# Kernel tuning notes

Hardware: AMD Instinct MI355X
Metric: run time of the kernel (lower is better)

## Reference

```python
import jax, jax.numpy as jnp
import numpy as np

N_NODES = 50000
N_EDGES = 800000
NFEAT, NHID, NCLASS = 128, 256, 64


def setup_inputs() -> dict:
    key = jax.random.key(0)
    ks = jax.random.split(key, 8)
    x = jax.random.normal(ks[0], (N_NODES, NFEAT), dtype=jnp.float32)
    edge_index = jax.random.randint(ks[1], (2, N_EDGES), 0, N_NODES, dtype=jnp.int64)
    s1 = 1.0 / np.sqrt(NFEAT)
    s2 = 1.0 / np.sqrt(NHID)
    W1_neigh = jax.random.normal(ks[2], (NFEAT, NHID), dtype=jnp.float32) * s1
    W1_root = jax.random.normal(ks[3], (NFEAT, NHID), dtype=jnp.float32) * s1
    b1 = jnp.zeros((NHID,), dtype=jnp.float32)
    W2_neigh = jax.random.normal(ks[4], (NHID, NCLASS), dtype=jnp.float32) * s2
    W2_root = jax.random.normal(ks[5], (NHID, NCLASS), dtype=jnp.float32) * s2
    b2 = jnp.zeros((NCLASS,), dtype=jnp.float32)
    return {"x": x, "edge_index": edge_index, "W1_neigh": W1_neigh,
            "W1_root": W1_root, "b1": b1, "W2_neigh": W2_neigh,
            "W2_root": W2_root, "b2": b2}


def _sage_conv(h, src, dst, n_nodes, W_neigh, W_root, b):
    # mean aggregation of source features into destination nodes
    msg = h[src]                                                   # [E, d]
    summed = jax.ops.segment_sum(msg, dst, num_segments=n_nodes)   # [N, d]
    cnt = jax.ops.segment_sum(jnp.ones((src.shape[0],), h.dtype), dst,
                              num_segments=n_nodes)                # [N]
    mean = summed / jnp.maximum(cnt, 1.0)[:, None]
    return mean @ W_neigh + h @ W_root + b


def reference(x, edge_index, W1_neigh, W1_root, b1, W2_neigh, W2_root, b2):
    src, dst = edge_index[0], edge_index[1]
    n = x.shape[0]
    h = jax.nn.relu(_sage_conv(x, src, dst, n, W1_neigh, W1_root, b1))
    # dropout is identity in eval mode
    out = _sage_conv(h, src, dst, n, W2_neigh, W2_root, b2)
    return out
```

## Files before the change

### kernel.cpp

```cpp
#include <hip/hip_runtime.h>

#define N_NODES 50000
#define N_EDGES 800000
#define NFEAT   128
#define NHID    256
#define NCLASS  64

#define NPASS 8
#define PASS_W ((N_NODES + NPASS - 1) / NPASS)
#define ECHUNK ((N_EDGES + 255) / 256)
#define ELLCAP 64

#define FILL_B (ECHUNK * NPASS)
#define CVTX_B ((N_NODES * 32 + 255) / 256)
#define CVTW_B (((65536 + 32768) + 255) / 256)

typedef unsigned short u16;
typedef unsigned int   u32;
typedef __attribute__((ext_vector_type(8))) u16   u16x8;
typedef __attribute__((ext_vector_type(8))) short s16x8;
typedef __attribute__((ext_vector_type(4))) float f32x4;

__device__ inline u16 f2bf(float f) {
    u32 u = __float_as_uint(f);
    u32 r = (u + 0x7FFFu + ((u >> 16) & 1u)) >> 16;
    return (u16)r;
}
__device__ inline float bflo(u32 v) { return __uint_as_float(v << 16); }
__device__ inline float bfhi(u32 v) { return __uint_as_float(v & 0xFFFF0000u); }

#define GLOAD_LDS16(g, l)                                                        \
    __builtin_amdgcn_global_load_lds(                                            \
        (const __attribute__((address_space(1))) u32*)(const void*)(g),          \
        (__attribute__((address_space(3))) u32*)(void*)(l), 16, 0, 0)

__global__ __launch_bounds__(256) void prep_fill_kernel(const float* __restrict__ x,
                                                        const int* __restrict__ ei,
                                                        const float* __restrict__ W1r,
                                                        const float* __restrict__ W1n,
                                                        const float* __restrict__ W2n,
                                                        const float* __restrict__ W2r,
                                                        u16* __restrict__ xa,
                                                        int* __restrict__ cnt,
                                                        int* __restrict__ ell,
                                                        u16* __restrict__ W1t,
                                                        u16* __restrict__ W2t) {
    int b = blockIdx.x;
    if (b < FILL_B) {
        int p = b & (NPASS - 1);
        int e = (b >> 3) * 256 + threadIdx.x;
        if (e >= N_EDGES) return;
        u32 d = (u32)ei[N_EDGES + e];
        u32 lo = (u32)(p * PASS_W);
        if (d - lo < (u32)PASS_W) {
            int s = ei[e];
            int pos = atomicAdd(&cnt[d], 1);
            if (pos < ELLCAP) ell[(size_t)d * ELLCAP + pos] = s;
        }
    } else if (b < FILL_B + CVTX_B) {
        int idx = (b - FILL_B) * 256 + threadIdx.x;
        if (idx >= N_NODES * 32) return;
        int r  = idx >> 5;
        int c4 = (idx & 31) * 4;
        float4 v = *reinterpret_cast<const float4*>(x + (size_t)r * NFEAT + c4);
        uint2 o;
        o.x = (u32)f2bf(v.x) | ((u32)f2bf(v.y) << 16);
        o.y = (u32)f2bf(v.z) | ((u32)f2bf(v.w) << 16);
        *reinterpret_cast<uint2*>(xa + (size_t)r * 256 + c4) = o;
    } else {
        int id = (b - FILL_B - CVTX_B) * 256 + threadIdx.x;
        if (id < 65536) {
            int k = id & 255, n = id >> 8;
            float v = (k < NFEAT) ? W1r[(size_t)k * NHID + n]
                                  : W1n[(size_t)(k - NFEAT) * NHID + n];
            W1t[(size_t)n * 256 + k] = f2bf(v);
        } else if (id < 65536 + 32768) {
            int j = id - 65536;
            int k = j & 255, n = j >> 8;
            float v = (n < NCLASS) ? W2n[(size_t)k * NCLASS + n]
                                   : W2r[(size_t)k * NCLASS + (n - NCLASS)];
            W2t[(size_t)n * 256 + k] = f2bf(v);
        }
    }
}

__global__ __launch_bounds__(256) void gather1_kernel(const int* __restrict__ cnt,
                                                      const int* __restrict__ ell,
                                                      u16* __restrict__ xa) {
    int gtid = blockIdx.x * 256 + threadIdx.x;
    int node = gtid >> 6;
    if (node >= N_NODES) return;
    int lane = threadIdx.x & 63;
    const u32* xrow = reinterpret_cast<const u32*>(xa);
    const int* idx = ell + (size_t)node * ELLCAP;
    int deg = cnt[node];
    if (deg > ELLCAP) deg = ELLCAP;
    float ax = 0.0f, ay = 0.0f;
    int j = 0;
    for (; j + 16 <= deg; j += 16) {
        int s[16]; u32 v[16];
        #pragma unroll
        for (int q = 0; q < 16; ++q) s[q] = idx[j + q];
        #pragma unroll
        for (int q = 0; q < 16; ++q) v[q] = xrow[(size_t)s[q] * 128 + lane];
        #pragma unroll
        for (int q = 0; q < 16; ++q) { ax += bflo(v[q]); ay += bfhi(v[q]); }
    }
    for (; j + 8 <= deg; j += 8) {
        int s[8]; u32 v[8];
        #pragma unroll
        for (int q = 0; q < 8; ++q) s[q] = idx[j + q];
        #pragma unroll
        for (int q = 0; q < 8; ++q) v[q] = xrow[(size_t)s[q] * 128 + lane];
        #pragma unroll
        for (int q = 0; q < 8; ++q) { ax += bflo(v[q]); ay += bfhi(v[q]); }
    }
    for (; j < deg; ++j) {
        u32 v = xrow[(size_t)idx[j] * 128 + lane];
        ax += bflo(v);
        ay += bfhi(v);
    }
    float invd = 1.0f / fmaxf((float)deg, 1.0f);
    u32 packed = (u32)f2bf(ax * invd) | ((u32)f2bf(ay * invd) << 16);
    reinterpret_cast<u32*>(xa + (size_t)node * 256 + 128)[lane] = packed;
}

__global__ __launch_bounds__(256) void gather2_kernel(const int* __restrict__ cnt,
                                                      const int* __restrict__ ell,
                                                      const u16* __restrict__ t,
                                                      float* __restrict__ out) {
    int gtid = blockIdx.x * 256 + threadIdx.x;
    int wave = gtid >> 6;
    int lane = threadIdx.x & 63;
    int node = wave * 2 + (lane >> 5);
    int l    = lane & 31;
    if (node >= N_NODES) return;
    const u32* trow = reinterpret_cast<const u32*>(t);
    const int* idx = ell + (size_t)node * ELLCAP;
    int deg = cnt[node];
    if (deg > ELLCAP) deg = ELLCAP;
    float ax = 0.0f, ay = 0.0f;
    int j = 0;
    for (; j + 16 <= deg; j += 16) {
        int s[16]; u32 v[16];
        #pragma unroll
        for (int q = 0; q < 16; ++q) s[q] = idx[j + q];
        #pragma unroll
        for (int q = 0; q < 16; ++q) v[q] = trow[(size_t)s[q] * 32 + l];
        #pragma unroll
        for (int q = 0; q < 16; ++q) { ax += bflo(v[q]); ay += bfhi(v[q]); }
    }
    for (; j + 8 <= deg; j += 8) {
        int s[8]; u32 v[8];
        #pragma unroll
        for (int q = 0; q < 8; ++q) s[q] = idx[j + q];
        #pragma unroll
        for (int q = 0; q < 8; ++q) v[q] = trow[(size_t)s[q] * 32 + l];
        #pragma unroll
        for (int q = 0; q < 8; ++q) { ax += bflo(v[q]); ay += bfhi(v[q]); }
    }
    for (; j < deg; ++j) {
        u32 v = trow[(size_t)idx[j] * 32 + l];
        ax += bflo(v); ay += bfhi(v);
    }
    float invd = 1.0f / fmaxf((float)deg, 1.0f);
    float* o = out + (size_t)node * NCLASS + l * 2;
    o[0] += ax * invd;
    o[1] += ay * invd;
}

__global__ __launch_bounds__(256) void gemm1_mfma(const u16* __restrict__ xa,
                                                  const u16* __restrict__ W1t,
                                                  const float* __restrict__ b1,
                                                  u16* __restrict__ h) {
    __shared__ u16 As[128 * 32];
    __shared__ u16 Bs[128 * 32];
    const int tid = threadIdx.x;
    const int r0 = blockIdx.x * 128;
    const int n0 = blockIdx.y * 128;
    const int wid = tid >> 6, ln = tid & 63;
    const int wm = (wid & 1) * 64, wn = (wid >> 1) * 64;
    const int lr = ln & 15;
    const int lq = ln >> 4;

    f32x4 acc[4][4] = {};

    for (int k0 = 0; k0 < 256; k0 += 32) {
        #pragma unroll
        for (int it = 0; it < 2; ++it) {
            int c   = it * 256 + tid;
            int row = c >> 2;
            int ko  = (c & 3) * 8;
            GLOAD_LDS16(xa  + (size_t)(r0 + row) * 256 + k0 + ko, As + c * 8);
            GLOAD_LDS16(W1t + (size_t)(n0 + row) * 256 + k0 + ko, Bs + c * 8);
        }
        __syncthreads();

        s16x8 af[4], bf[4];
        #pragma unroll
        for (int i = 0; i < 4; ++i)
            af[i] = *reinterpret_cast<const s16x8*>(As + (wm + i * 16 + lr) * 32 + lq * 8);
        #pragma unroll
        for (int j = 0; j < 4; ++j)
            bf[j] = *reinterpret_cast<const s16x8*>(Bs + (wn + j * 16 + lr) * 32 + lq * 8);
        #pragma unroll
        for (int i = 0; i < 4; ++i)
            #pragma unroll
            for (int j = 0; j < 4; ++j)
                acc[i][j] = __builtin_amdgcn_mfma_f32_16x16x32_bf16(af[i], bf[j], acc[i][j], 0, 0, 0);
        __syncthreads();
    }

    #pragma unroll
    for (int i = 0; i < 4; ++i) {
        #pragma unroll
        for (int j = 0; j < 4; ++j) {
            int col = n0 + wn + j * 16 + lr;
            float bias = b1[col];
            #pragma unroll
            for (int r = 0; r < 4; ++r) {
                int row = r0 + wm + i * 16 + lq * 4 + r;
                if (row < N_NODES)
                    h[(size_t)row * 256 + col] = f2bf(fmaxf(acc[i][j][r] + bias, 0.0f));
            }
        }
    }
}

__global__ __launch_bounds__(256) void gemm2_mfma(const u16* __restrict__ h,
                                                  const u16* __restrict__ W2t,
                                                  const float* __restrict__ b2,
                                                  u16* __restrict__ t,
                                                  float* __restrict__ out) {
    __shared__ u16 As[128 * 32];
    __shared__ u16 Bs[128 * 32];
    const int tid = threadIdx.x;
    const int r0 = blockIdx.x * 128;
    const int wid = tid >> 6, ln = tid & 63;
    const int wm = (wid & 1) * 64, wn = (wid >> 1) * 64;
    const int lr = ln & 15;
    const int lq = ln >> 4;

    f32x4 acc[4][4] = {};

    for (int k0 = 0; k0 < 256; k0 += 32) {
        #pragma unroll
        for (int it = 0; it < 2; ++it) {
            int c   = it * 256 + tid;
            int row = c >> 2;
            int ko  = (c & 3) * 8;
            GLOAD_LDS16(h   + (size_t)(r0 + row) * 256 + k0 + ko, As + c * 8);
            GLOAD_LDS16(W2t + (size_t)row * 256 + k0 + ko,        Bs + c * 8);
        }
        __syncthreads();

        s16x8 af[4], bf[4];
        #pragma unroll
        for (int i = 0; i < 4; ++i)
            af[i] = *reinterpret_cast<const s16x8*>(As + (wm + i * 16 + lr) * 32 + lq * 8);
        #pragma unroll
        for (int j = 0; j < 4; ++j)
            bf[j] = *reinterpret_cast<const s16x8*>(Bs + (wn + j * 16 + lr) * 32 + lq * 8);
        #pragma unroll
        for (int i = 0; i < 4; ++i)
            #pragma unroll
            for (int j = 0; j < 4; ++j)
                acc[i][j] = __builtin_amdgcn_mfma_f32_16x16x32_bf16(af[i], bf[j], acc[i][j], 0, 0, 0);
        __syncthreads();
    }

    #pragma unroll
    for (int i = 0; i < 4; ++i) {
        #pragma unroll
        for (int j = 0; j < 4; ++j) {
            int col = wn + j * 16 + lr;
            #pragma unroll
            for (int r = 0; r < 4; ++r) {
                int row = r0 + wm + i * 16 + lq * 4 + r;
                if (row >= N_NODES) continue;
                if (col < NCLASS) {
                    t[(size_t)row * NCLASS + col] = f2bf(acc[i][j][r]);
                } else {
                    int c = col - NCLASS;
                    out[(size_t)row * NCLASS + c] = acc[i][j][r] + b2[c];
                }
            }
        }
    }
}

extern "C" void kernel_launch(void* const* d_in, const int* in_sizes, int n_in,
                              void* d_out, int out_size, void* d_ws, size_t ws_size,
                              hipStream_t stream) {
    const float* x    = (const float*)d_in[0];
    const int*   ei   = (const int*)d_in[1];
    const float* W1n  = (const float*)d_in[2];
    const float* W1r  = (const float*)d_in[3];
    const float* b1   = (const float*)d_in[4];
    const float* W2n  = (const float*)d_in[5];
    const float* W2r  = (const float*)d_in[6];
    const float* b2   = (const float*)d_in[7];
    float* out = (float*)d_out;

    int* cnt = (int*)d_ws;
    int* ell = cnt + 50048;
    u16* xa  = (u16*)(ell + (size_t)N_NODES * ELLCAP);
    u16* h   = xa + (size_t)N_NODES * 256;
    u16* t   = h  + (size_t)N_NODES * 256;
    u16* W1t = t  + (size_t)N_NODES * 64;
    u16* W2t = W1t + 65536;

    hipMemsetAsync(cnt, 0, 50048 * sizeof(int), stream);

    prep_fill_kernel<<<FILL_B + CVTX_B + CVTW_B, 256, 0, stream>>>(
        x, ei, W1r, W1n, W2n, W2r, xa, cnt, ell, W1t, W2t);

    gather1_kernel<<<(N_NODES * 64 + 255) / 256, 256, 0, stream>>>(cnt, ell, xa);
    gemm1_mfma<<<dim3((N_NODES + 127) / 128, 2), 256, 0, stream>>>(xa, W1t, b1, h);

    gemm2_mfma<<<(N_NODES + 127) / 128, 256, 0, stream>>>(h, W2t, b2, t, out);
    gather2_kernel<<<(N_NODES * 32 + 255) / 256, 256, 0, stream>>>(cnt, ell, t, out);
}
```

Measured before the change: 230.2 us.

## Widen gemm1 tile to full output width and pair edges in ELL fill

The first GEMM now computes all 256 output columns per block (128x256 tile, 4x8 MFMA accumulators per wave) instead of splitting the columns across two blocks. Each A tile is loaded once rather than twice, but register pressure and LDS use double and the grid halves. The ELL fill also handles two edges per thread with int2 loads, which cuts the number of threads and load instructions in the multi-pass scatter.

```diff
diff --git a/kernel.cpp b/kernel.cpp
--- a/kernel.cpp
+++ b/kernel.cpp
@@ -8,12 +8,13 @@
 
 #define NPASS 8
 #define PASS_W ((N_NODES + NPASS - 1) / NPASS)
-#define ECHUNK ((N_EDGES + 255) / 256)
 #define ELLCAP 64
 
-#define FILL_B (ECHUNK * NPASS)
-#define CVTX_B ((N_NODES * 32 + 255) / 256)
-#define CVTW_B (((65536 + 32768) + 255) / 256)
+#define NPAIR   (N_EDGES / 2)
+#define ECHUNK2 ((NPAIR + 255) / 256)
+#define FILL_B  (ECHUNK2 * NPASS)
+#define CVTX_B  ((N_NODES * 32 + 255) / 256)
+#define CVTW_B  (((65536 + 32768) + 255) / 256)
 
 typedef unsigned short u16;
 typedef unsigned int   u32;
@@ -48,14 +49,22 @@
     int b = blockIdx.x;
     if (b < FILL_B) {
         int p = b & (NPASS - 1);
-        int e = (b >> 3) * 256 + threadIdx.x;
-        if (e >= N_EDGES) return;
-        u32 d = (u32)ei[N_EDGES + e];
+        int i = (b >> 3) * 256 + threadIdx.x;
+        if (i >= NPAIR) return;
+        int2 d2 = reinterpret_cast<const int2*>(ei + N_EDGES)[i];
         u32 lo = (u32)(p * PASS_W);
-        if (d - lo < (u32)PASS_W) {
-            int s = ei[e];
-            int pos = atomicAdd(&cnt[d], 1);
-            if (pos < ELLCAP) ell[(size_t)d * ELLCAP + pos] = s;
+        bool in0 = ((u32)d2.x - lo) < (u32)PASS_W;
+        bool in1 = ((u32)d2.y - lo) < (u32)PASS_W;
+        if (in0 | in1) {
+            int2 s2 = reinterpret_cast<const int2*>(ei)[i];
+            if (in0) {
+                int pos = atomicAdd(&cnt[d2.x], 1);
+                if (pos < ELLCAP) ell[(size_t)d2.x * ELLCAP + pos] = s2.x;
+            }
+            if (in1) {
+                int pos = atomicAdd(&cnt[d2.y], 1);
+                if (pos < ELLCAP) ell[(size_t)d2.y * ELLCAP + pos] = s2.y;
+            }
         }
     } else if (b < FILL_B + CVTX_B) {
         int idx = (b - FILL_B) * 256 + threadIdx.x;
@@ -174,16 +183,15 @@
                                                   const float* __restrict__ b1,
                                                   u16* __restrict__ h) {
     __shared__ u16 As[128 * 32];
-    __shared__ u16 Bs[128 * 32];
+    __shared__ u16 Bs[256 * 32];
     const int tid = threadIdx.x;
     const int r0 = blockIdx.x * 128;
-    const int n0 = blockIdx.y * 128;
     const int wid = tid >> 6, ln = tid & 63;
-    const int wm = (wid & 1) * 64, wn = (wid >> 1) * 64;
+    const int wm = (wid & 1) * 64, wn = (wid >> 1) * 128;
     const int lr = ln & 15;
     const int lq = ln >> 4;
 
-    f32x4 acc[4][4] = {};
+    f32x4 acc[4][8] = {};
 
     for (int k0 = 0; k0 < 256; k0 += 32) {
         #pragma unroll
@@ -191,22 +199,28 @@
             int c   = it * 256 + tid;
             int row = c >> 2;
             int ko  = (c & 3) * 8;
-            GLOAD_LDS16(xa  + (size_t)(r0 + row) * 256 + k0 + ko, As + c * 8);
-            GLOAD_LDS16(W1t + (size_t)(n0 + row) * 256 + k0 + ko, Bs + c * 8);
+            GLOAD_LDS16(xa + (size_t)(r0 + row) * 256 + k0 + ko, As + c * 8);
+        }
+        #pragma unroll
+        for (int it = 0; it < 4; ++it) {
+            int c   = it * 256 + tid;
+            int row = c >> 2;
+            int ko  = (c & 3) * 8;
+            GLOAD_LDS16(W1t + (size_t)row * 256 + k0 + ko, Bs + c * 8);
         }
         __syncthreads();
 
-        s16x8 af[4], bf[4];
+        s16x8 af[4], bf[8];
         #pragma unroll
         for (int i = 0; i < 4; ++i)
             af[i] = *reinterpret_cast<const s16x8*>(As + (wm + i * 16 + lr) * 32 + lq * 8);
         #pragma unroll
-        for (int j = 0; j < 4; ++j)
+        for (int j = 0; j < 8; ++j)
             bf[j] = *reinterpret_cast<const s16x8*>(Bs + (wn + j * 16 + lr) * 32 + lq * 8);
         #pragma unroll
         for (int i = 0; i < 4; ++i)
             #pragma unroll
-            for (int j = 0; j < 4; ++j)
+            for (int j = 0; j < 8; ++j)
                 acc[i][j] = __builtin_amdgcn_mfma_f32_16x16x32_bf16(af[i], bf[j], acc[i][j], 0, 0, 0);
         __syncthreads();
     }
@@ -214,8 +228,8 @@
     #pragma unroll
     for (int i = 0; i < 4; ++i) {
         #pragma unroll
-        for (int j = 0; j < 4; ++j) {
-            int col = n0 + wn + j * 16 + lr;
+        for (int j = 0; j < 8; ++j) {
+            int col = wn + j * 16 + lr;
             float bias = b1[col];
             #pragma unroll
             for (int r = 0; r < 4; ++r) {
@@ -316,7 +330,7 @@
         x, ei, W1r, W1n, W2n, W2r, xa, cnt, ell, W1t, W2t);
 
     gather1_kernel<<<(N_NODES * 64 + 255) / 256, 256, 0, stream>>>(cnt, ell, xa);
-    gemm1_mfma<<<dim3((N_NODES + 127) / 128, 2), 256, 0, stream>>>(xa, W1t, b1, h);
+    gemm1_mfma<<<(N_NODES + 127) / 128, 256, 0, stream>>>(xa, W1t, b1, h);
 
     gemm2_mfma<<<(N_NODES + 127) / 128, 256, 0, stream>>>(h, W2t, b2, t, out);
     gather2_kernel<<<(N_NODES * 32 + 255) / 256, 256, 0, stream>>>(cnt, ell, t, out);
```

New measurement: 239.8 us. +4.2%, slower.
